# Kernel optimization log

Measured on AMD Instinct MI355X. Metric: run time of the kernel, lower is better.

Reference implementation:

```python
import jax, jax.numpy as jnp
import numpy as np

B, H, W, C = 4, 64, 64, 64


def conv1x1(x, w, b):
    # 1x1 conv on channels_last input == per-pixel dense layer
    return jnp.einsum('bhwc,cd->bhwd', x, w) + b


def setup_inputs() -> dict:
    key = jax.random.key(0)
    ks = jax.random.split(key, 8)
    std = 1.0 / np.sqrt(C)
    inp = {
        'x': jax.random.normal(ks[0], (B, H, W, C), dtype=jnp.float32),
        'wq_s': jax.random.normal(ks[1], (C, C), dtype=jnp.float32) * std,
        'bq_s': jnp.zeros((C,), jnp.float32),
        'wk_s': jax.random.normal(ks[2], (C, C), dtype=jnp.float32) * std,
        'bk_s': jnp.zeros((C,), jnp.float32),
        'wv_s': jax.random.normal(ks[3], (C, C), dtype=jnp.float32) * std,
        'bv_s': jnp.zeros((C,), jnp.float32),
        'wq_c': jax.random.normal(ks[4], (C, C), dtype=jnp.float32) * std,
        'bq_c': jnp.zeros((C,), jnp.float32),
        'wk_c': jax.random.normal(ks[5], (C, C), dtype=jnp.float32) * std,
        'bk_c': jnp.zeros((C,), jnp.float32),
        'wv_c': jax.random.normal(ks[6], (C, C), dtype=jnp.float32) * std,
        'bv_c': jnp.zeros((C,), jnp.float32),
        'a': jnp.float32(0.0),
        'b': jnp.float32(0.0),
    }
    return inp


def reference(x, wq_s, bq_s, wk_s, bk_s, wv_s, bv_s,
              wq_c, bq_c, wk_c, bk_c, wv_c, bv_c, a, b):
    scale = jnp.sqrt(jnp.float32(C))
    N = H * W

    # ---- Spatial self-attention: tokens = pixels, (B, HW, C) ----
    qs = conv1x1(x, wq_s, bq_s).reshape(B, N, C)
    ks_ = conv1x1(x, wk_s, bk_s).reshape(B, N, C)
    vs = conv1x1(x, wv_s, bv_s).reshape(B, N, C)
    att_s = jax.nn.softmax(jnp.einsum('bnc,bmc->bnm', qs, ks_) / scale, axis=-1)
    spat = jnp.einsum('bnm,bmc->bnc', att_s, vs).reshape(B, H, W, C)

    # ---- Channel self-attention ----
    # Faithful to the TF code: raw reshape of channels_last (B,H,W,C) -> (B,C,HW)
    # (a memory reinterpretation, NOT a transpose).
    qc = conv1x1(x, wq_c, bq_c).reshape(B, C, N)
    kc = conv1x1(x, wk_c, bk_c).reshape(B, C, N)
    vc = conv1x1(x, wv_c, bv_c).reshape(B, C, N)
    att_c = jax.nn.softmax(jnp.einsum('bcn,bdn->bcd', qc, kc) / scale, axis=-1)
    chan = jnp.einsum('bcd,bdn->bcn', att_c, vc).reshape(B, H, W, C)

    # ---- Scaled residual fusion ----
    return (b * spat + x) + (a * chan + x)
```

## Files before the change

### kernel.cpp

```cpp
#include <hip/hip_runtime.h>

#define NTOK 4096
#define PSTR 72

typedef short bf16x8 __attribute__((ext_vector_type(8)));
typedef short bf16x4 __attribute__((ext_vector_type(4)));
typedef float f32x4 __attribute__((ext_vector_type(4)));

__device__ __forceinline__ short f2bf(float f) {
  union { float f; unsigned u; } v; v.f = f;
  unsigned r = v.u + 0x7fffu + ((v.u >> 16) & 1u);
  return (short)(r >> 16);
}
__device__ __forceinline__ short f2bf_t(float f) {
  union { float f; unsigned u; } v; v.f = f;
  return (short)(v.u >> 16);
}
__device__ __forceinline__ float bf2f(short s) {
  union { unsigned u; float f; } v; v.u = ((unsigned)(unsigned short)s) << 16;
  return v.f;
}

struct PrepArgs {
  const float* w[6];
  short* wt;
};

struct ConvArgs {
  const float* x;
  const short* wt;
  const float* bias[6];
  short* out[6];
};

#define QSC (0.125f * 1.44269504088896f)

__global__ __launch_bounds__(256) void prep_w(PrepArgs p) {
  const int wi = blockIdx.x;
  const float* w = p.w[wi];
  short* o = p.wt + wi*4096;
  const int d = threadIdx.x & 63, cb = (threadIdx.x >> 6) * 16;
  const float sc = (wi == 0) ? QSC : 1.f;
  bf16x8 v0, v1;
  for (int j=0;j<8;j++) {
    v0[j] = f2bf(w[(cb+j)*64 + d] * sc);
    v1[j] = f2bf(w[(cb+8+j)*64 + d] * sc);
  }
  *(bf16x8*)(o + d*64 + cb)     = v0;
  *(bf16x8*)(o + d*64 + cb + 8) = v1;
}

__global__ __launch_bounds__(256) void conv_qkv(ConvArgs args) {
  __shared__ __align__(16) short lT[64*PSTR];
  const int tid = threadIdx.x;
  const int wave = tid >> 6, lane = tid & 63;
  const int quad = lane >> 4, l16 = lane & 15;

  int row = blockIdx.x * 64 + wave*16 + l16;
  const float* xr = args.x + (size_t)row*64 + quad*8;
  f32x4 x0 = *(const f32x4*)xr;
  f32x4 x1 = *(const f32x4*)(xr+4);
  f32x4 x2 = *(const f32x4*)(xr+32);
  f32x4 x3 = *(const f32x4*)(xr+36);
  bf16x8 a0, a1;
  for (int j=0;j<4;j++){ a0[j]=f2bf(x0[j]); a0[4+j]=f2bf(x1[j]); a1[j]=f2bf(x2[j]); a1[4+j]=f2bf(x3[j]); }

  int orow_base = blockIdx.x*64 + wave*16 + quad*4;
  for (int wi=0; wi<6; wi++) {
    const short* wtp = args.wt + wi*4096;
    for (int dt=0; dt<4; dt++) {
      bf16x8 b0 = *(const bf16x8*)(wtp + (dt*16+l16)*64 + quad*8);
      bf16x8 b1 = *(const bf16x8*)(wtp + (dt*16+l16)*64 + 32 + quad*8);
      f32x4 acc = {0.f,0.f,0.f,0.f};
      acc = __builtin_amdgcn_mfma_f32_16x16x32_bf16(a0, b0, acc, 0,0,0);
      acc = __builtin_amdgcn_mfma_f32_16x16x32_bf16(a1, b1, acc, 0,0,0);
      float bias = args.bias[wi][dt*16+l16];
      if (wi == 0) bias *= QSC;
      if (wi != 2) {
        short* outp = args.out[wi];
        for (int r=0;r<4;r++)
          outp[(size_t)(orow_base + r)*64 + dt*16 + l16] = f2bf(acc[r] + bias);
      } else {
        for (int r=0;r<4;r++)
          lT[(dt*16+l16)*PSTR + wave*16 + quad*4 + r] = f2bf(acc[r] + bias);
      }
    }
  }
  __syncthreads();
  int b  = (blockIdx.x*64) >> 12;
  int n0 = (blockIdx.x*64) & 4095;
  for (int u0=0; u0<2; u0++) {
    int u = u0*256 + tid;
    int c = u >> 3, t8 = u & 7;
    *(bf16x8*)(args.out[2] + (size_t)(b*64+c)*4096 + n0 + t8*8) =
        *(const bf16x8*)&lT[c*PSTR + t8*8];
  }
}

__global__ __launch_bounds__(256, 3) void attn_part(const short* __restrict__ qs,
    const short* __restrict__ ks, const short* __restrict__ vst,
    short* __restrict__ opart, float* __restrict__ ml) {
  __shared__ __align__(16) short sK[2][64*PSTR];
  __shared__ __align__(16) short sV[2][64*PSTR];
  __shared__ __align__(16) short sP[4][16*PSTR];
  const int tid = threadIdx.x;
  const int wave = tid>>6, lane = tid&63, quad = lane>>4, l16 = lane&15;
  const int qtile = blockIdx.x*2 + (wave>>1);
  const int qgo = (wave&1)*2;
  const int batch = blockIdx.y, kg = blockIdx.z;
  const int srow = tid >> 3, sc8 = tid & 7;

  const short* kb  = ks  + (size_t)batch*NTOK*64;
  const short* vtb = vst + (size_t)batch*64*NTOK;
  const int k0base = kg*512;

  bf16x8 qa[2][2];
  for (int qg=0;qg<2;qg++) {
    const short* qp = qs + ((size_t)batch*NTOK + qtile*64 + (qgo+qg)*16 + l16)*64;
    qa[qg][0] = *(const bf16x8*)(qp + quad*8);
    qa[qg][1] = *(const bf16x8*)(qp + 32 + quad*8);
  }

  f32x4 ot[2][4];
  for (int qg=0;qg<2;qg++) for (int ct=0;ct<4;ct++) ot[qg][ct]=(f32x4){0.f,0.f,0.f,0.f};
  float lq[2] = {0.f,0.f};

  for (int h=0;h<2;h++) {
    int row = (h*256+tid)>>3, c8 = (h*256+tid)&7;
    *(bf16x8*)&sK[0][row*PSTR + c8*8] = *(const bf16x8*)(kb + (size_t)(k0base+row)*64 + c8*8);
    *(bf16x8*)&sV[0][row*PSTR + c8*8] = *(const bf16x8*)(vtb + (size_t)row*4096 + k0base + c8*8);
  }
  __syncthreads();

  for (int t=0; t<8; t++) {
    const int cur = t & 1;
    bf16x8 gk0, gk1, gv0, gv1;
    if (t < 7) {
      int k0 = k0base + (t+1)*64;
      gk0 = *(const bf16x8*)(kb + (size_t)(k0+srow)*64 + sc8*8);
      gv0 = *(const bf16x8*)(vtb + (size_t)srow*4096 + k0 + sc8*8);
      gk1 = *(const bf16x8*)(kb + (size_t)(k0+32+srow)*64 + sc8*8);
      gv1 = *(const bf16x8*)(vtb + (size_t)(32+srow)*4096 + k0 + sc8*8);
    }

    bf16x8 kf[4][2], vf[4][2];
    for (int mt=0;mt<4;mt++) {
      kf[mt][0] = *(const bf16x8*)&sK[cur][(mt*16+l16)*PSTR + quad*8];
      kf[mt][1] = *(const bf16x8*)&sK[cur][(mt*16+l16)*PSTR + 32 + quad*8];
      vf[mt][0] = *(const bf16x8*)&sV[cur][(mt*16+l16)*PSTR + quad*8];
      vf[mt][1] = *(const bf16x8*)&sV[cur][(mt*16+l16)*PSTR + 32 + quad*8];
    }

    for (int qg=0;qg<2;qg++) {
      f32x4 st[4];
      for (int mt=0;mt<4;mt++) {
        f32x4 z = {0.f,0.f,0.f,0.f};
        z = __builtin_amdgcn_mfma_f32_16x16x32_bf16(kf[mt][0], qa[qg][0], z, 0,0,0);
        z = __builtin_amdgcn_mfma_f32_16x16x32_bf16(kf[mt][1], qa[qg][1], z, 0,0,0);
        st[mt] = z;
      }
      float sum = 0.f;
      for (int mt=0;mt<4;mt++)
        for (int r=0;r<4;r++) {
          float p = __builtin_amdgcn_exp2f(st[mt][r]);
          st[mt][r] = p; sum += p;
        }
      lq[qg] += sum;
      short* lPw = sP[wave];
      for (int mt=0;mt<4;mt++) {
        bf16x4 pk;
        for (int r=0;r<4;r++) pk[r] = f2bf_t(st[mt][r]);
        *(bf16x4*)&lPw[l16*PSTR + mt*16 + quad*4] = pk;
      }
      bf16x8 pb0 = *(const bf16x8*)&lPw[l16*PSTR + quad*8];
      bf16x8 pb1 = *(const bf16x8*)&lPw[l16*PSTR + 32 + quad*8];
      for (int ct=0;ct<4;ct++) {
        ot[qg][ct] = __builtin_amdgcn_mfma_f32_16x16x32_bf16(vf[ct][0], pb0, ot[qg][ct], 0,0,0);
        ot[qg][ct] = __builtin_amdgcn_mfma_f32_16x16x32_bf16(vf[ct][1], pb1, ot[qg][ct], 0,0,0);
      }
    }

    if (t < 7) {
      int nxt = cur ^ 1;
      *(bf16x8*)&sK[nxt][srow*PSTR + sc8*8]      = gk0;
      *(bf16x8*)&sV[nxt][srow*PSTR + sc8*8]      = gv0;
      *(bf16x8*)&sK[nxt][(32+srow)*PSTR + sc8*8] = gk1;
      *(bf16x8*)&sV[nxt][(32+srow)*PSTR + sc8*8] = gv1;
    }
    __syncthreads();
  }

  size_t obase = (((size_t)batch*64 + qtile)*8 + kg) * 4096;
  for (int qg=0;qg<2;qg++)
    for (int ct=0;ct<4;ct++) {
      bf16x4 pk;
      for (int r=0;r<4;r++) pk[r] = f2bf(ot[qg][ct][r]);
      *(bf16x4*)&opart[obase + (size_t)((qgo+qg)*1024 + ct*256 + quad*64 + l16*4)] = pk;
    }
  float lt[2];
  for (int qg=0;qg<2;qg++) {
    float s = lq[qg];
    s += __shfl_xor(s, 16);
    s += __shfl_xor(s, 32);
    lt[qg] = s;
  }
  if (quad == 0) {
    float* mlp = ml + (((size_t)batch*64 + qtile)*8 + kg)*64;
    for (int qg=0;qg<2;qg++)
      mlp[(qgo+qg)*16 + l16] = lt[qg];
  }
}

__global__ __launch_bounds__(256) void chan_qk_part(const short* __restrict__ qc,
    const short* __restrict__ kc, float* __restrict__ Gpart) {
  const int tid = threadIdx.x;
  const int wave = tid>>6, lane = tid&63, quad = lane>>4, l16 = lane&15;
  const int ks_ = blockIdx.x, b = blockIdx.y;
  const int n0 = ks_*64;
  const short* qb = qc + (size_t)b*NTOK*64;
  const short* kb = kc + (size_t)b*NTOK*64;

  bf16x8 aq0 = *(const bf16x8*)(qb + (size_t)(wave*16+l16)*4096 + n0 + quad*8);
  bf16x8 aq1 = *(const bf16x8*)(qb + (size_t)(wave*16+l16)*4096 + n0 + 32 + quad*8);
  f32x4 acc[4];
  for (int nt=0;nt<4;nt++) {
    bf16x8 bk0 = *(const bf16x8*)(kb + (size_t)(nt*16+l16)*4096 + n0 + quad*8);
    bf16x8 bk1 = *(const bf16x8*)(kb + (size_t)(nt*16+l16)*4096 + n0 + 32 + quad*8);
    f32x4 z = {0.f,0.f,0.f,0.f};
    z = __builtin_amdgcn_mfma_f32_16x16x32_bf16(aq0, bk0, z, 0,0,0);
    z = __builtin_amdgcn_mfma_f32_16x16x32_bf16(aq1, bk1, z, 0,0,0);
    acc[nt] = z;
  }
  float* gp = Gpart + ((size_t)b*64 + ks_)*4096;
  for (int nt=0;nt<4;nt++)
    for (int r=0;r<4;r++)
      gp[(wave*16 + quad*4 + r)*64 + nt*16 + l16] = acc[nt][r];
}

__global__ __launch_bounds__(256) void chan_reduce_sm(const float* __restrict__ Gpart,
    float* __restrict__ att) {
  const int cg = blockIdx.x, b = blockIdx.y, t = threadIdx.x;
  const int c = cg*16 + (t>>4), dq = t & 15;
  const float* gp = Gpart + (size_t)b*64*4096 + c*64 + dq*4;
  f32x4 acc = {0.f,0.f,0.f,0.f};
  for (int ks_=0; ks_<64; ks_++)
    acc += *(const f32x4*)(gp + (size_t)ks_*4096);
  const float SC = 0.125f * 1.44269504088896f;
  f32x4 v;
  for (int j=0;j<4;j++) v[j] = acc[j]*SC;
  float mx = fmaxf(fmaxf(v[0],v[1]), fmaxf(v[2],v[3]));
  mx = fmaxf(mx, __shfl_xor(mx, 1));
  mx = fmaxf(mx, __shfl_xor(mx, 2));
  mx = fmaxf(mx, __shfl_xor(mx, 4));
  mx = fmaxf(mx, __shfl_xor(mx, 8));
  f32x4 p; float sum = 0.f;
  for (int j=0;j<4;j++){ p[j] = __builtin_amdgcn_exp2f(v[j]-mx); sum += p[j]; }
  sum += __shfl_xor(sum, 1);
  sum += __shfl_xor(sum, 2);
  sum += __shfl_xor(sum, 4);
  sum += __shfl_xor(sum, 8);
  float inv = 1.f/sum;
  f32x4 r; for (int j=0;j<4;j++) r[j] = p[j]*inv;
  *(f32x4*)(att + (size_t)b*4096 + c*64 + dq*4) = r;
}

__global__ __launch_bounds__(256) void combine_fuse(const short* __restrict__ opart,
    const float* __restrict__ ml, const float* __restrict__ att,
    const short* __restrict__ vc, const float* __restrict__ x,
    const float* __restrict__ pa, const float* __restrict__ pb,
    float* __restrict__ out) {
  __shared__ float sInv[64];
  __shared__ float sAtt[64];
  const int qt = blockIdx.x, b = blockIdx.y, hz = blockIdx.z, t = threadIdx.x;
  const size_t base = ((size_t)b*64 + qt)*8;
  if (t < 64) {
    float den = 0.f;
    for (int kg=0;kg<8;kg++) den += ml[(base+kg)*64 + t];
    sInv[t] = 1.f/den;
    sAtt[t] = att[(size_t)b*4096 + qt*64 + t];
  }
  __syncthreads();

  const int e0 = hz*2048 + t*8;
  const int q = e0 >> 6;
  const int qg = q >> 4, l16 = q & 15;
  const int seg = (t&7) >> 1, quad0 = (t&1)*2;

  float accS[8];
  for (int j=0;j<8;j++) accS[j]=0.f;
  for (int kg=0;kg<8;kg++) {
    const short* op = opart + (base+kg)*4096 + qg*1024 + seg*256 + l16*4;
    bf16x4 c0 = *(const bf16x4*)(op + quad0*64);
    bf16x4 c1 = *(const bf16x4*)(op + (quad0+1)*64);
    for (int r=0;r<4;r++) { accS[r] += bf2f(c0[r]); accS[4+r] += bf2f(c1[r]); }
  }
  float inv = sInv[q];
  float accC[8];
  for (int j=0;j<8;j++) accC[j]=0.f;
  const short* vb = vc + (size_t)b*NTOK*64;
  for (int d=0; d<64; d++) {
    bf16x8 v = *(const bf16x8*)(vb + (size_t)d*4096 + e0);
    float a = sAtt[d];
    for (int j=0;j<8;j++) accC[j] += a*bf2f(v[j]);
  }
  const float av = pa[0], bv = pb[0];
  size_t flat = ((size_t)b*64 + qt)*4096 + e0;
  f32x4 x0 = *(const f32x4*)(x + flat);
  f32x4 x1 = *(const f32x4*)(x + flat + 4);
  f32x4 r0, r1;
  for (int j=0;j<4;j++) {
    r0[j] = bv*accS[j]*inv   + av*accC[j]   + 2.f*x0[j];
    r1[j] = bv*accS[4+j]*inv + av*accC[4+j] + 2.f*x1[j];
  }
  *(f32x4*)(out + flat)     = r0;
  *(f32x4*)(out + flat + 4) = r1;
}

extern "C" void kernel_launch(void* const* d_in, const int* in_sizes, int n_in,
                              void* d_out, int out_size, void* d_ws, size_t ws_size,
                              hipStream_t stream) {
  const float* x = (const float*)d_in[0];
  char* ws = (char*)d_ws;
  const size_t MB = 1048576;
  short* qs    = (short*)(ws + 0*MB);
  short* ks_   = (short*)(ws + 2*MB);
  short* vst   = (short*)(ws + 4*MB);
  short* qc    = (short*)(ws + 6*MB);
  short* kc    = (short*)(ws + 8*MB);
  short* vc    = (short*)(ws + 10*MB);
  short* opart = (short*)(ws + 12*MB);
  float* ml    = (float*)(ws + 28*MB);
  float* att   = (float*)(ws + 29*MB);
  short* wt    = (short*)(ws + 30*MB);
  float* Gpart = (float*)(ws + 0*MB);

  PrepArgs pa;
  ConvArgs ca;
  ca.x = x; ca.wt = wt;
  for (int i=0;i<6;i++) {
    pa.w[i]    = (const float*)d_in[1+2*i];
    ca.bias[i] = (const float*)d_in[2+2*i];
  }
  pa.wt = wt;
  ca.out[0]=qs; ca.out[1]=ks_; ca.out[2]=vst;
  ca.out[3]=qc; ca.out[4]=kc; ca.out[5]=vc;

  hipLaunchKernelGGL(prep_w, dim3(6), dim3(256), 0, stream, pa);
  hipLaunchKernelGGL(conv_qkv, dim3(256), dim3(256), 0, stream, ca);
  hipLaunchKernelGGL(attn_part, dim3(32,4,8), dim3(256), 0, stream, qs, ks_, vst, opart, ml);
  hipLaunchKernelGGL(chan_qk_part, dim3(64,4), dim3(256), 0, stream, qc, kc, Gpart);
  hipLaunchKernelGGL(chan_reduce_sm, dim3(4,4), dim3(256), 0, stream, Gpart, att);
  hipLaunchKernelGGL(combine_fuse, dim3(64,4,2), dim3(256), 0, stream,
                     opart, ml, att, vc, x, (const float*)d_in[13], (const float*)d_in[14],
                     (float*)d_out);
}
```

Measured before the change: 142.9 us.

## Split conv across two block halves, rebalance attention key split, fuse channel softmax

The QKV projection kernel now launches twice as many blocks, each computing three of the six projections, and the channel-query scale is folded into the weights. The spatial attention splits keys into 6 uneven groups (11 or 10 tiles) instead of 8, so 768 blocks are launched instead of 1024, which should better match the machine's concurrent capacity and shrinks the partial outputs that must be combined. The separate channel-softmax reduction kernel is removed and its work moves into the combine kernel's prologue, dropping one launch. The cost is that every combine block redundantly sums 64 Gpart partials, and the uneven key split creates a small load imbalance.

```diff
diff --git a/kernel.cpp b/kernel.cpp
--- a/kernel.cpp
+++ b/kernel.cpp
@@ -40,7 +40,7 @@
   const float* w = p.w[wi];
   short* o = p.wt + wi*4096;
   const int d = threadIdx.x & 63, cb = (threadIdx.x >> 6) * 16;
-  const float sc = (wi == 0) ? QSC : 1.f;
+  const float sc = (wi == 0 || wi == 3) ? QSC : 1.f;
   bf16x8 v0, v1;
   for (int j=0;j<8;j++) {
     v0[j] = f2bf(w[(cb+j)*64 + d] * sc);
@@ -55,6 +55,7 @@
   const int tid = threadIdx.x;
   const int wave = tid >> 6, lane = tid & 63;
   const int quad = lane >> 4, l16 = lane & 15;
+  const int half = blockIdx.y;
 
   int row = blockIdx.x * 64 + wave*16 + l16;
   const float* xr = args.x + (size_t)row*64 + quad*8;
@@ -66,7 +67,8 @@
   for (int j=0;j<4;j++){ a0[j]=f2bf(x0[j]); a0[4+j]=f2bf(x1[j]); a1[j]=f2bf(x2[j]); a1[4+j]=f2bf(x3[j]); }
 
   int orow_base = blockIdx.x*64 + wave*16 + quad*4;
-  for (int wi=0; wi<6; wi++) {
+  for (int j=0; j<3; j++) {
+    const int wi = half*3 + j;
     const short* wtp = args.wt + wi*4096;
     for (int dt=0; dt<4; dt++) {
       bf16x8 b0 = *(const bf16x8*)(wtp + (dt*16+l16)*64 + quad*8);
@@ -75,7 +77,7 @@
       acc = __builtin_amdgcn_mfma_f32_16x16x32_bf16(a0, b0, acc, 0,0,0);
       acc = __builtin_amdgcn_mfma_f32_16x16x32_bf16(a1, b1, acc, 0,0,0);
       float bias = args.bias[wi][dt*16+l16];
-      if (wi == 0) bias *= QSC;
+      if (wi == 0 || wi == 3) bias *= QSC;
       if (wi != 2) {
         short* outp = args.out[wi];
         for (int r=0;r<4;r++)
@@ -86,14 +88,16 @@
       }
     }
   }
-  __syncthreads();
-  int b  = (blockIdx.x*64) >> 12;
-  int n0 = (blockIdx.x*64) & 4095;
-  for (int u0=0; u0<2; u0++) {
-    int u = u0*256 + tid;
-    int c = u >> 3, t8 = u & 7;
-    *(bf16x8*)(args.out[2] + (size_t)(b*64+c)*4096 + n0 + t8*8) =
-        *(const bf16x8*)&lT[c*PSTR + t8*8];
+  if (half == 0) {
+    __syncthreads();
+    int b  = (blockIdx.x*64) >> 12;
+    int n0 = (blockIdx.x*64) & 4095;
+    for (int u0=0; u0<2; u0++) {
+      int u = u0*256 + tid;
+      int c = u >> 3, t8 = u & 7;
+      *(bf16x8*)(args.out[2] + (size_t)(b*64+c)*4096 + n0 + t8*8) =
+          *(const bf16x8*)&lT[c*PSTR + t8*8];
+    }
   }
 }
 
@@ -109,10 +113,11 @@
   const int qgo = (wave&1)*2;
   const int batch = blockIdx.y, kg = blockIdx.z;
   const int srow = tid >> 3, sc8 = tid & 7;
+  const int ntile  = (kg < 4) ? 11 : 10;
+  const int k0base = ((kg < 4) ? kg*11 : 44 + (kg-4)*10) * 64;
 
   const short* kb  = ks  + (size_t)batch*NTOK*64;
   const short* vtb = vst + (size_t)batch*64*NTOK;
-  const int k0base = kg*512;
 
   bf16x8 qa[2][2];
   for (int qg=0;qg<2;qg++) {
@@ -132,10 +137,11 @@
   }
   __syncthreads();
 
-  for (int t=0; t<8; t++) {
+  for (int t=0; t<ntile; t++) {
     const int cur = t & 1;
     bf16x8 gk0, gk1, gv0, gv1;
-    if (t < 7) {
+    const bool pf = (t+1 < ntile);
+    if (pf) {
       int k0 = k0base + (t+1)*64;
       gk0 = *(const bf16x8*)(kb + (size_t)(k0+srow)*64 + sc8*8);
       gv0 = *(const bf16x8*)(vtb + (size_t)srow*4096 + k0 + sc8*8);
@@ -180,7 +186,7 @@
       }
     }
 
-    if (t < 7) {
+    if (pf) {
       int nxt = cur ^ 1;
       *(bf16x8*)&sK[nxt][srow*PSTR + sc8*8]      = gk0;
       *(bf16x8*)&sV[nxt][srow*PSTR + sc8*8]      = gv0;
@@ -190,7 +196,7 @@
     __syncthreads();
   }
 
-  size_t obase = (((size_t)batch*64 + qtile)*8 + kg) * 4096;
+  size_t obase = (((size_t)batch*64 + qtile)*6 + kg) * 4096;
   for (int qg=0;qg<2;qg++)
     for (int ct=0;ct<4;ct++) {
       bf16x4 pk;
@@ -205,7 +211,7 @@
     lt[qg] = s;
   }
   if (quad == 0) {
-    float* mlp = ml + (((size_t)batch*64 + qtile)*8 + kg)*64;
+    float* mlp = ml + (((size_t)batch*64 + qtile)*6 + kg)*64;
     for (int qg=0;qg<2;qg++)
       mlp[(qgo+qg)*16 + l16] = lt[qg];
   }
@@ -237,47 +243,28 @@
       gp[(wave*16 + quad*4 + r)*64 + nt*16 + l16] = acc[nt][r];
 }
 
-__global__ __launch_bounds__(256) void chan_reduce_sm(const float* __restrict__ Gpart,
-    float* __restrict__ att) {
-  const int cg = blockIdx.x, b = blockIdx.y, t = threadIdx.x;
-  const int c = cg*16 + (t>>4), dq = t & 15;
-  const float* gp = Gpart + (size_t)b*64*4096 + c*64 + dq*4;
-  f32x4 acc = {0.f,0.f,0.f,0.f};
-  for (int ks_=0; ks_<64; ks_++)
-    acc += *(const f32x4*)(gp + (size_t)ks_*4096);
-  const float SC = 0.125f * 1.44269504088896f;
-  f32x4 v;
-  for (int j=0;j<4;j++) v[j] = acc[j]*SC;
-  float mx = fmaxf(fmaxf(v[0],v[1]), fmaxf(v[2],v[3]));
-  mx = fmaxf(mx, __shfl_xor(mx, 1));
-  mx = fmaxf(mx, __shfl_xor(mx, 2));
-  mx = fmaxf(mx, __shfl_xor(mx, 4));
-  mx = fmaxf(mx, __shfl_xor(mx, 8));
-  f32x4 p; float sum = 0.f;
-  for (int j=0;j<4;j++){ p[j] = __builtin_amdgcn_exp2f(v[j]-mx); sum += p[j]; }
-  sum += __shfl_xor(sum, 1);
-  sum += __shfl_xor(sum, 2);
-  sum += __shfl_xor(sum, 4);
-  sum += __shfl_xor(sum, 8);
-  float inv = 1.f/sum;
-  f32x4 r; for (int j=0;j<4;j++) r[j] = p[j]*inv;
-  *(f32x4*)(att + (size_t)b*4096 + c*64 + dq*4) = r;
-}
-
 __global__ __launch_bounds__(256) void combine_fuse(const short* __restrict__ opart,
-    const float* __restrict__ ml, const float* __restrict__ att,
+    const float* __restrict__ ml, const float* __restrict__ Gpart,
     const short* __restrict__ vc, const float* __restrict__ x,
     const float* __restrict__ pa, const float* __restrict__ pb,
     float* __restrict__ out) {
   __shared__ float sInv[64];
   __shared__ float sAtt[64];
   const int qt = blockIdx.x, b = blockIdx.y, hz = blockIdx.z, t = threadIdx.x;
-  const size_t base = ((size_t)b*64 + qt)*8;
+  const size_t base6 = ((size_t)b*64 + qt)*6;
   if (t < 64) {
     float den = 0.f;
-    for (int kg=0;kg<8;kg++) den += ml[(base+kg)*64 + t];
+    for (int kg=0;kg<6;kg++) den += ml[(base6+kg)*64 + t];
     sInv[t] = 1.f/den;
-    sAtt[t] = att[(size_t)b*4096 + qt*64 + t];
+    float g = 0.f;
+    const float* gp = Gpart + (size_t)b*64*4096 + qt*64 + t;
+    for (int ks=0; ks<64; ks++) g += gp[(size_t)ks*4096];
+    float m = g;
+    for (int off=1; off<64; off<<=1) m = fmaxf(m, __shfl_xor(m, off));
+    float p = __builtin_amdgcn_exp2f(g - m);
+    float s = p;
+    for (int off=1; off<64; off<<=1) s += __shfl_xor(s, off);
+    sAtt[t] = p/s;
   }
   __syncthreads();
 
@@ -288,8 +275,8 @@
 
   float accS[8];
   for (int j=0;j<8;j++) accS[j]=0.f;
-  for (int kg=0;kg<8;kg++) {
-    const short* op = opart + (base+kg)*4096 + qg*1024 + seg*256 + l16*4;
+  for (int kg=0;kg<6;kg++) {
+    const short* op = opart + (base6+kg)*4096 + qg*1024 + seg*256 + l16*4;
     bf16x4 c0 = *(const bf16x4*)(op + quad0*64);
     bf16x4 c1 = *(const bf16x4*)(op + (quad0+1)*64);
     for (int r=0;r<4;r++) { accS[r] += bf2f(c0[r]); accS[4+r] += bf2f(c1[r]); }
@@ -329,9 +316,8 @@
   short* kc    = (short*)(ws + 8*MB);
   short* vc    = (short*)(ws + 10*MB);
   short* opart = (short*)(ws + 12*MB);
-  float* ml    = (float*)(ws + 28*MB);
-  float* att   = (float*)(ws + 29*MB);
-  short* wt    = (short*)(ws + 30*MB);
+  float* ml    = (float*)(ws + 24*MB);
+  short* wt    = (short*)(ws + 25*MB);
   float* Gpart = (float*)(ws + 0*MB);
 
   PrepArgs pa;
@@ -346,11 +332,10 @@
   ca.out[3]=qc; ca.out[4]=kc; ca.out[5]=vc;
 
   hipLaunchKernelGGL(prep_w, dim3(6), dim3(256), 0, stream, pa);
-  hipLaunchKernelGGL(conv_qkv, dim3(256), dim3(256), 0, stream, ca);
-  hipLaunchKernelGGL(attn_part, dim3(32,4,8), dim3(256), 0, stream, qs, ks_, vst, opart, ml);
+  hipLaunchKernelGGL(conv_qkv, dim3(256,2), dim3(256), 0, stream, ca);
+  hipLaunchKernelGGL(attn_part, dim3(32,4,6), dim3(256), 0, stream, qs, ks_, vst, opart, ml);
   hipLaunchKernelGGL(chan_qk_part, dim3(64,4), dim3(256), 0, stream, qc, kc, Gpart);
-  hipLaunchKernelGGL(chan_reduce_sm, dim3(4,4), dim3(256), 0, stream, Gpart, att);
   hipLaunchKernelGGL(combine_fuse, dim3(64,4,2), dim3(256), 0, stream,
-                     opart, ml, att, vc, x, (const float*)d_in[13], (const float*)d_in[14],
+                     opart, ml, Gpart, vc, x, (const float*)d_in[13], (const float*)d_in[14],
                      (float*)d_out);
 }
```

New measurement: 140.7 us. No clear change (-1.6%).
